# Kernel tuning notes

Measured on AMD Instinct MI355X. Metric: run time of the kernel, lower is better.

Reference implementation:

```python
import jax, jax.numpy as jnp
import numpy as np

N_V = 50000
N_E = 800000
IN = 128
OUT = 128
ADD_SELF_LOOPS = True


def setup_inputs() -> dict:
    key = jax.random.key(0)
    ks = jax.random.split(key, 7)
    x = jax.random.normal(ks[0], (N_V, IN), dtype=jnp.float32)
    # random edges, avoiding self-loops (src != dst) to match a simple graph
    src = jax.random.randint(ks[1], (N_E,), 0, N_V, dtype=jnp.int32)
    off = jax.random.randint(ks[2], (N_E,), 1, N_V, dtype=jnp.int32)
    dst = (src + off) % N_V
    edge_index = jnp.stack([src, dst], axis=0)  # [2, N_E]
    # edge_w_builder: Linear(2*IN, OUT) + Tanh   (torch default uniform init)
    s1 = 1.0 / float(np.sqrt(2 * IN))
    W_edge = jax.random.uniform(ks[3], (2 * IN, OUT), jnp.float32, -s1, s1)
    b_edge = jax.random.uniform(ks[4], (OUT,), jnp.float32, -s1, s1)
    # lin: Linear(IN, OUT, bias=False)
    s2 = 1.0 / float(np.sqrt(IN))
    W_lin = jax.random.uniform(ks[5], (IN, OUT), jnp.float32, -s2, s2)
    bias = jax.random.uniform(ks[6], (OUT,), jnp.float32, -s2, s2)
    return {"x": x, "edge_index": edge_index, "W_edge": W_edge,
            "b_edge": b_edge, "W_lin": W_lin, "bias": bias}


def reference(x, edge_index, W_edge, b_edge, W_lin, bias):
    # The sheaf construction uses indices (src*OUT+c, dst*OUT+c): strictly
    # channel-diagonal blocks. The Hadamard product L * (E + I) therefore
    # reduces per-edge-per-channel:
    #   off-diag (u,w in E0):  (-norm_uw) * s_ec
    #   diagonal (v,v):        (1 - 1/d_v) * 1   (self-loops added),
    # and solver = I - L*(E+I) gives
    #   off-diag: +norm_uw * s_ec,   diag: 1/d_v.
    src, dst = edge_index[0], edge_index[1]
    # edge MLP: tanh(Linear(cat(x_src, x_dst)))  -> [N_E, OUT]
    sheaf_w = jnp.tanh(jnp.concatenate([x[src], x[dst]], axis=1) @ W_edge + b_edge)
    # symmetric-normalized Laplacian weights over graph with self-loops
    deg = jax.ops.segment_sum(jnp.ones((N_E,), x.dtype), src, num_segments=N_V)
    if ADD_SELF_LOOPS:
        deg = deg + 1.0
    dinv = jnp.where(deg > 0, jax.lax.rsqrt(deg), 0.0)  # D^{-1/2}
    norm = dinv[src] * dinv[dst]                        # [N_E]
    x_lin = x @ W_lin                                   # [N_V, OUT]
    # out[v,c] = diag_v * x_lin[v,c] + sum_{e: src=v} norm_e * s_ec * x_lin[dst_e,c]
    msgs = (norm[:, None] * sheaf_w) * x_lin[dst]       # [N_E, OUT]
    agg = jax.ops.segment_sum(msgs, src, num_segments=N_V)
    diag = (dinv * dinv)[:, None] if ADD_SELF_LOOPS else jnp.zeros((N_V, 1), x.dtype)
    out = diag * x_lin + agg + bias
    return out, sheaf_w
```

## Files before the change

### kernel.cpp

```cpp
#include <hip/hip_runtime.h>
#include <hip/hip_bf16.h>

#define NV 50000
#define NE 800000
#define C  128
#define CAP 80
#define NBV ((NV + 255) / 256)

typedef __attribute__((ext_vector_type(8))) short short8;
typedef __attribute__((ext_vector_type(4))) float f32x4;

__device__ __forceinline__ float fast_tanh(float v) {
    float av = fabsf(v);
    float t  = __expf(-2.0f * av);
    float r  = (1.0f - t) * __builtin_amdgcn_rcpf(1.0f + t);
    return copysignf(r, v);
}

__device__ __forceinline__ unsigned short f2bf(float f) {
    __hip_bfloat16 h = __float2bfloat16(f);
    return reinterpret_cast<unsigned short&>(h);
}
__device__ __forceinline__ float bflo(unsigned u) { return __uint_as_float(u << 16); }
__device__ __forceinline__ float bfhi(unsigned u) { return __uint_as_float(u & 0xffff0000u); }

__device__ __forceinline__ void nt_store_f2(float2* p, float2 v) {
    union { float2 f; unsigned long long u; } c; c.f = v;
    __builtin_nontemporal_store(c.u, (unsigned long long*)p);
}

__device__ __forceinline__ float lane_bcast_f(float x, int l) {
    return __uint_as_float((unsigned)__builtin_amdgcn_readlane((int)__float_as_uint(x), l));
}

__global__ __launch_bounds__(256) void k_zero(int* cur) {
    int v = blockIdx.x * 256 + threadIdx.x;
    if (v < NV) cur[v] = 0;
}

__global__ __launch_bounds__(256) void k_fillb(
    const int* __restrict__ src, const int* __restrict__ dst,
    int* cur, unsigned long long* __restrict__ bkt) {
    int e = blockIdx.x * 256 + threadIdx.x;
    if (e >= NE) return;
    int s = src[e];
    int p = atomicAdd(&cur[s], 1);
    if (p < CAP)
        bkt[(size_t)s * CAP + p] =
            ((unsigned long long)(unsigned)dst[e] << 32) | (unsigned)e;
}

__global__ __launch_bounds__(256) void k_prep(
    const int* __restrict__ cur, float* __restrict__ dinv,
    const float* __restrict__ We, const float* __restrict__ Wl,
    unsigned short* __restrict__ Wt) {
    if (blockIdx.x < NBV) {
        int v = blockIdx.x * 256 + threadIdx.x;
        if (v < NV) dinv[v] = rsqrtf((float)cur[v] + 1.0f);
    } else {
        int gid = (blockIdx.x - NBV) * 256 + threadIdx.x;
        if (gid >= 384 * 128) return;
        int n = gid >> 7, k = gid & 127;
        float v;
        if      (n < 128) v = We[(size_t)k * C + n];
        else if (n < 256) v = We[(size_t)(128 + k) * C + (n - 128)];
        else              v = Wl[(size_t)k * C + (n - 256)];
        Wt[(size_t)n * 128 + k] = f2bf(v);
    }
}

__global__ __launch_bounds__(256) void gemm_mfma(
    const float* __restrict__ x, const unsigned short* __restrict__ Wt,
    const float* __restrict__ be,
    float* __restrict__ A, uint2* __restrict__ BX2)
{
    __shared__ unsigned short xs[128 * 128];
    const int tid  = threadIdx.x;
    const int row0 = blockIdx.x * 128;

    #pragma unroll
    for (int i = 0; i < 8; ++i) {
        int L   = tid + i * 256;
        int row = L >> 4;
        int c   = L & 15;
        int grow = row0 + row;
        float4 f0 = make_float4(0.f,0.f,0.f,0.f), f1 = f0;
        if (grow < NV) {
            const float* p = x + (size_t)grow * C + c * 8;
            f0 = *(const float4*)p;
            f1 = *(const float4*)(p + 4);
        }
        unsigned short r[8];
        r[0]=f2bf(f0.x); r[1]=f2bf(f0.y); r[2]=f2bf(f0.z); r[3]=f2bf(f0.w);
        r[4]=f2bf(f1.x); r[5]=f2bf(f1.y); r[6]=f2bf(f1.z); r[7]=f2bf(f1.w);
        *(uint4*)(&xs[row * 128 + (c ^ (row & 7)) * 8]) = *(uint4*)r;
    }
    __syncthreads();

    const int w    = tid >> 6;
    const int lane = tid & 63;
    const int col  = lane & 15;
    const int kgrp = lane >> 4;

    auto compute_ct = [&](int ct, f32x4 acc[2]) {
        acc[0] = (f32x4){0.f, 0.f, 0.f, 0.f};
        acc[1] = (f32x4){0.f, 0.f, 0.f, 0.f};
        const int n = ct * 16 + col;
        #pragma unroll
        for (int kt = 0; kt < 4; ++kt) {
            const int k0 = kt * 32 + kgrp * 8;
            short8 b = *(const short8*)(Wt + (size_t)n * 128 + k0);
            #pragma unroll
            for (int rs = 0; rs < 2; ++rs) {
                int row = w * 32 + rs * 16 + col;
                int cc  = (k0 >> 3) ^ (row & 7);
                short8 a = *(const short8*)(&xs[row * 128 + cc * 8]);
                acc[rs] = __builtin_amdgcn_mfma_f32_16x16x32_bf16(a, b, acc[rs], 0, 0, 0);
            }
        }
    };

    for (int ct = 0; ct < 8; ++ct) {
        f32x4 acc[2];
        compute_ct(ct, acc);
        const int nn = ct * 16 + col;
        const float bv = be[nn];
        #pragma unroll
        for (int rs = 0; rs < 2; ++rs)
            #pragma unroll
            for (int r = 0; r < 4; ++r) {
                int grow = row0 + w * 32 + rs * 16 + kgrp * 4 + r;
                if (grow < NV) A[(size_t)grow * C + nn] = acc[rs][r] + bv;
            }
    }

    for (int p = 0; p < 8; ++p) {
        f32x4 accb[2], accx[2];
        compute_ct(8 + p,  accb);
        compute_ct(16 + p, accx);
        const int half = p * 8 + (col >> 1);
        #pragma unroll
        for (int rs = 0; rs < 2; ++rs)
            #pragma unroll
            for (int r = 0; r < 4; ++r) {
                float ob = accb[rs][r], pb = __shfl_xor(ob, 1);
                float ox = accx[rs][r], px = __shfl_xor(ox, 1);
                if (!(lane & 1)) {
                    int grow = row0 + w * 32 + rs * 16 + kgrp * 4 + r;
                    if (grow < NV) {
                        uint2 pk;
                        pk.x = (unsigned)f2bf(ob) | ((unsigned)f2bf(pb) << 16);
                        pk.y = (unsigned)f2bf(ox) | ((unsigned)f2bf(px) << 16);
                        BX2[(size_t)grow * 64 + half] = pk;
                    }
                }
            }
    }
}

__global__ __launch_bounds__(256) void k_gather(
    const int* __restrict__ cnt, const unsigned long long* __restrict__ bkt,
    const float* __restrict__ dinv, const float* __restrict__ A,
    const uint2* __restrict__ BX, const float* __restrict__ bias,
    float* __restrict__ out, float* __restrict__ sheaf)
{
    int v = blockIdx.x * 4 + (threadIdx.x >> 6);
    if (v >= NV) return;
    int lane = threadIdx.x & 63;

    float2* S2 = (float2*)sheaf;

    float  di = dinv[v];
    float2 a  = ((const float2*)A)[(size_t)v * 64 + lane];
    uint2  pv = BX[(size_t)v * 64 + lane];
    float2 b2 = ((const float2*)bias)[lane];
    float  dd = di * di;
    float accx = dd * bflo(pv.y) + b2.x;
    float accy = dd * bfhi(pv.y) + b2.y;

    int deg = cnt[v]; if (deg > CAP) deg = CAP;
    const unsigned long long* eb = bkt + (size_t)v * CAP;

    for (int base = 0; base < deg; base += 64) {
        int nb = deg - base; if (nb > 64) nb = 64;
        int myd = 0, mye = 0; float dn = 0.f;
        if (lane < nb) {
            unsigned long long pk = eb[base + lane];
            myd = (int)(pk >> 32);
            mye = (int)(pk & 0xffffffffull);
            dn  = di * dinv[myd];
        }

        uint2 q[8]; int ed[8]; float nr[8];

        auto loadg = [&](int jj, uint2* qq, int* ee, float* nn) {
            #pragma unroll
            for (int u = 0; u < 8; ++u) {
                int d  = __builtin_amdgcn_readlane(myd, jj + u);
                ee[u]  = __builtin_amdgcn_readlane(mye, jj + u);
                nn[u]  = lane_bcast_f(dn, jj + u);
                qq[u]  = BX[(size_t)(unsigned)d * 64 + lane];
            }
        };
        auto computeg = [&](uint2* qq, int* ee, float* nn) {
            #pragma unroll
            for (int u = 0; u < 8; ++u) {
                float2 sv;
                sv.x = fast_tanh(a.x + bflo(qq[u].x));
                sv.y = fast_tanh(a.y + bfhi(qq[u].x));
                nt_store_f2(&S2[(size_t)(unsigned)ee[u] * 64 + lane], sv);
                accx += nn[u] * sv.x * bflo(qq[u].y);
                accy += nn[u] * sv.y * bfhi(qq[u].y);
            }
        };

        int j = 0;
        if (j + 8 <= nb) {
            loadg(0, q, ed, nr);
            for (; j + 16 <= nb; j += 8) {
                uint2 q2[8]; int ed2[8]; float nr2[8];
                loadg(j + 8, q2, ed2, nr2);
                computeg(q, ed, nr);
                #pragma unroll
                for (int u = 0; u < 8; ++u) { q[u] = q2[u]; ed[u] = ed2[u]; nr[u] = nr2[u]; }
            }
            computeg(q, ed, nr);
            j += 8;
        }
        for (; j + 4 <= nb; j += 4) {
            uint2 qq[4]; int ee[4]; float nn[4];
            #pragma unroll
            for (int u = 0; u < 4; ++u) {
                int d  = __builtin_amdgcn_readlane(myd, j + u);
                ee[u]  = __builtin_amdgcn_readlane(mye, j + u);
                nn[u]  = lane_bcast_f(dn, j + u);
                qq[u]  = BX[(size_t)(unsigned)d * 64 + lane];
            }
            #pragma unroll
            for (int u = 0; u < 4; ++u) {
                float2 sv;
                sv.x = fast_tanh(a.x + bflo(qq[u].x));
                sv.y = fast_tanh(a.y + bfhi(qq[u].x));
                nt_store_f2(&S2[(size_t)(unsigned)ee[u] * 64 + lane], sv);
                accx += nn[u] * sv.x * bflo(qq[u].y);
                accy += nn[u] * sv.y * bfhi(qq[u].y);
            }
        }
        for (; j < nb; ++j) {
            int d   = __builtin_amdgcn_readlane(myd, j);
            int e   = __builtin_amdgcn_readlane(mye, j);
            float nrm = lane_bcast_f(dn, j);
            uint2 qq = BX[(size_t)(unsigned)d * 64 + lane];
            float2 sv;
            sv.x = fast_tanh(a.x + bflo(qq.x));
            sv.y = fast_tanh(a.y + bfhi(qq.x));
            nt_store_f2(&S2[(size_t)(unsigned)e * 64 + lane], sv);
            accx += nrm * sv.x * bflo(qq.y);
            accy += nrm * sv.y * bfhi(qq.y);
        }
    }
    float2 o; o.x = accx; o.y = accy;
    nt_store_f2(&((float2*)out)[(size_t)v * 64 + lane], o);
}

extern "C" void kernel_launch(void* const* d_in, const int* in_sizes, int n_in,
                              void* d_out, int out_size, void* d_ws, size_t ws_size,
                              hipStream_t stream) {
    const float* x    = (const float*)d_in[0];
    const int*   ei   = (const int*)  d_in[1];
    const float* We   = (const float*)d_in[2];
    const float* be   = (const float*)d_in[3];
    const float* Wl   = (const float*)d_in[4];
    const float* bias = (const float*)d_in[5];

    float* out   = (float*)d_out;
    float* sheaf = out + (size_t)NV * C;

    const int* src = ei;
    const int* dst = ei + NE;

    char* wsb = (char*)d_ws;
    const size_t SEG = 256 * 1024;
    int*   cur  = (int*)(wsb);
    float* dinv = (float*)(wsb + SEG);
    unsigned long long* bkt = (unsigned long long*)(wsb + 2 * SEG);
    char*  after = wsb + 2 * SEG + (size_t)NV * CAP * 8;
    float* A  = (float*)after;
    uint2* BX = (uint2*)(A + (size_t)NV * C);
    unsigned short* Wt = (unsigned short*)(BX + (size_t)NV * 64);

    k_zero  <<<(NV + 255) / 256, 256, 0, stream>>>(cur);
    k_fillb <<<(NE + 255) / 256, 256, 0, stream>>>(src, dst, cur, bkt);
    k_prep  <<<NBV + (384 * 128 + 255) / 256, 256, 0, stream>>>(cur, dinv, We, Wl, Wt);
    gemm_mfma<<<(NV + 127) / 128, 256, 0, stream>>>(x, Wt, be, A, BX);
    k_gather<<<(NV + 3) / 4, 256, 0, stream>>>(cur, bkt, dinv, A, BX, bias, out, sheaf);
}
```

Measured before the change: 217.1 us.

## Merge zero and weight-prep kernels, compute dinv on the fly, use nontemporal loads

Merges the counter-zeroing kernel with the weight transpose/convert kernel and removes the separate dinv kernel. Degree normalisation is now recomputed in the gather kernel from the counts, using rsqrt of count plus one. Edge indices, x rows and bucket entries are read with nontemporal loads. This cuts one kernel launch and the dinv buffer, at the cost of an extra rsqrt per edge in the gather.

```diff
diff --git a/kernel.cpp b/kernel.cpp
--- a/kernel.cpp
+++ b/kernel.cpp
@@ -9,6 +9,7 @@
 
 typedef __attribute__((ext_vector_type(8))) short short8;
 typedef __attribute__((ext_vector_type(4))) float f32x4;
+typedef __attribute__((ext_vector_type(4))) unsigned int u32x4;
 
 __device__ __forceinline__ float fast_tanh(float v) {
     float av = fabsf(v);
@@ -28,35 +29,21 @@
     union { float2 f; unsigned long long u; } c; c.f = v;
     __builtin_nontemporal_store(c.u, (unsigned long long*)p);
 }
+__device__ __forceinline__ float4 nt_load_f4(const float* p) {
+    u32x4 u = __builtin_nontemporal_load((const u32x4*)p);
+    union { u32x4 u; float4 f; } c; c.u = u; return c.f;
+}
 
 __device__ __forceinline__ float lane_bcast_f(float x, int l) {
     return __uint_as_float((unsigned)__builtin_amdgcn_readlane((int)__float_as_uint(x), l));
 }
 
-__global__ __launch_bounds__(256) void k_zero(int* cur) {
-    int v = blockIdx.x * 256 + threadIdx.x;
-    if (v < NV) cur[v] = 0;
-}
-
-__global__ __launch_bounds__(256) void k_fillb(
-    const int* __restrict__ src, const int* __restrict__ dst,
-    int* cur, unsigned long long* __restrict__ bkt) {
-    int e = blockIdx.x * 256 + threadIdx.x;
-    if (e >= NE) return;
-    int s = src[e];
-    int p = atomicAdd(&cur[s], 1);
-    if (p < CAP)
-        bkt[(size_t)s * CAP + p] =
-            ((unsigned long long)(unsigned)dst[e] << 32) | (unsigned)e;
-}
-
-__global__ __launch_bounds__(256) void k_prep(
-    const int* __restrict__ cur, float* __restrict__ dinv,
-    const float* __restrict__ We, const float* __restrict__ Wl,
+__global__ __launch_bounds__(256) void k_init(
+    int* cur, const float* __restrict__ We, const float* __restrict__ Wl,
     unsigned short* __restrict__ Wt) {
     if (blockIdx.x < NBV) {
         int v = blockIdx.x * 256 + threadIdx.x;
-        if (v < NV) dinv[v] = rsqrtf((float)cur[v] + 1.0f);
+        if (v < NV) cur[v] = 0;
     } else {
         int gid = (blockIdx.x - NBV) * 256 + threadIdx.x;
         if (gid >= 384 * 128) return;
@@ -69,6 +56,19 @@
     }
 }
 
+__global__ __launch_bounds__(256) void k_fillb(
+    const int* __restrict__ src, const int* __restrict__ dst,
+    int* cur, unsigned long long* __restrict__ bkt) {
+    int e = blockIdx.x * 256 + threadIdx.x;
+    if (e >= NE) return;
+    int s = __builtin_nontemporal_load(src + e);
+    int d = __builtin_nontemporal_load(dst + e);
+    int p = atomicAdd(&cur[s], 1);
+    if (p < CAP)
+        bkt[(size_t)s * CAP + p] =
+            ((unsigned long long)(unsigned)d << 32) | (unsigned)e;
+}
+
 __global__ __launch_bounds__(256) void gemm_mfma(
     const float* __restrict__ x, const unsigned short* __restrict__ Wt,
     const float* __restrict__ be,
@@ -87,8 +87,8 @@
         float4 f0 = make_float4(0.f,0.f,0.f,0.f), f1 = f0;
         if (grow < NV) {
             const float* p = x + (size_t)grow * C + c * 8;
-            f0 = *(const float4*)p;
-            f1 = *(const float4*)(p + 4);
+            f0 = nt_load_f4(p);
+            f1 = nt_load_f4(p + 4);
         }
         unsigned short r[8];
         r[0]=f2bf(f0.x); r[1]=f2bf(f0.y); r[2]=f2bf(f0.z); r[3]=f2bf(f0.w);
@@ -160,7 +160,7 @@
 
 __global__ __launch_bounds__(256) void k_gather(
     const int* __restrict__ cnt, const unsigned long long* __restrict__ bkt,
-    const float* __restrict__ dinv, const float* __restrict__ A,
+    const float* __restrict__ A,
     const uint2* __restrict__ BX, const float* __restrict__ bias,
     float* __restrict__ out, float* __restrict__ sheaf)
 {
@@ -170,7 +170,8 @@
 
     float2* S2 = (float2*)sheaf;
 
-    float  di = dinv[v];
+    int    cv = cnt[v];
+    float  di = rsqrtf((float)cv + 1.0f);
     float2 a  = ((const float2*)A)[(size_t)v * 64 + lane];
     uint2  pv = BX[(size_t)v * 64 + lane];
     float2 b2 = ((const float2*)bias)[lane];
@@ -178,17 +179,17 @@
     float accx = dd * bflo(pv.y) + b2.x;
     float accy = dd * bfhi(pv.y) + b2.y;
 
-    int deg = cnt[v]; if (deg > CAP) deg = CAP;
+    int deg = cv; if (deg > CAP) deg = CAP;
     const unsigned long long* eb = bkt + (size_t)v * CAP;
 
     for (int base = 0; base < deg; base += 64) {
         int nb = deg - base; if (nb > 64) nb = 64;
         int myd = 0, mye = 0; float dn = 0.f;
         if (lane < nb) {
-            unsigned long long pk = eb[base + lane];
+            unsigned long long pk = __builtin_nontemporal_load(eb + base + lane);
             myd = (int)(pk >> 32);
             mye = (int)(pk & 0xffffffffull);
-            dn  = di * dinv[myd];
+            dn  = di * rsqrtf((float)cnt[myd] + 1.0f);
         }
 
         uint2 q[8]; int ed[8]; float nr[8];
@@ -282,16 +283,14 @@
     char* wsb = (char*)d_ws;
     const size_t SEG = 256 * 1024;
     int*   cur  = (int*)(wsb);
-    float* dinv = (float*)(wsb + SEG);
     unsigned long long* bkt = (unsigned long long*)(wsb + 2 * SEG);
     char*  after = wsb + 2 * SEG + (size_t)NV * CAP * 8;
     float* A  = (float*)after;
     uint2* BX = (uint2*)(A + (size_t)NV * C);
     unsigned short* Wt = (unsigned short*)(BX + (size_t)NV * 64);
 
-    k_zero  <<<(NV + 255) / 256, 256, 0, stream>>>(cur);
+    k_init  <<<NBV + (384 * 128 + 255) / 256, 256, 0, stream>>>(cur, We, Wl, Wt);
     k_fillb <<<(NE + 255) / 256, 256, 0, stream>>>(src, dst, cur, bkt);
-    k_prep  <<<NBV + (384 * 128 + 255) / 256, 256, 0, stream>>>(cur, dinv, We, Wl, Wt);
     gemm_mfma<<<(NV + 127) / 128, 256, 0, stream>>>(x, Wt, be, A, BX);
-    k_gather<<<(NV + 3) / 4, 256, 0, stream>>>(cur, bkt, dinv, A, BX, bias, out, sheaf);
-}
+    k_gather<<<(NV + 3) / 4, 256, 0, stream>>>(cur, bkt, A, BX, bias, out, sheaf);
+}
```

Result: no change. 215.4 us (-0.8%).
